# Kernel tuning notes

Measured on AMD Instinct MI355X. Metric: run time of the kernel, lower is better.

## Reference

```python
import jax, jax.numpy as jnp
import numpy as np

N_CAT, IN, HID, VOCAB, B = 512, 1536, 2048, 32000, 256
C = N_CAT + IN + HID  # cell_size = 4096


def setup_inputs() -> dict:
    key = jax.random.key(0)
    ks = jax.random.split(key, 16)
    s = 1.0 / np.sqrt(C)
    inp = {
        "category": jax.random.normal(ks[0], (B, N_CAT), jnp.float32),
        "x": jax.random.normal(ks[1], (B, IN), jnp.float32),
        "hidden": jax.random.normal(ks[2], (B, HID), jnp.float32),
        "cell": jnp.zeros((B, C), jnp.float32),
        # gate weights, torch Linear layout [out, in]
        "Wf": jax.random.uniform(ks[3], (C, C), jnp.float32, -s, s),
        "bf": jax.random.uniform(ks[4], (C,), jnp.float32, -s, s),
        "Wi": jax.random.uniform(ks[5], (C, C), jnp.float32, -s, s),
        "bi": jax.random.uniform(ks[6], (C,), jnp.float32, -s, s),
        "Wc": jax.random.uniform(ks[7], (C, C), jnp.float32, -s, s),
        "bc": jax.random.uniform(ks[8], (C,), jnp.float32, -s, s),
        "Wo": jax.random.uniform(ks[9], (C, C), jnp.float32, -s, s),
        "bo": jax.random.uniform(ks[10], (C,), jnp.float32, -s, s),
        "Wout": jax.random.uniform(ks[11], (VOCAB, C), jnp.float32, -s, s),
        "bout": jax.random.uniform(ks[12], (VOCAB,), jnp.float32, -s, s),
    }
    return inp


def reference(category, x, hidden, cell, Wf, bf, Wi, bi, Wc, bc, Wo, bo, Wout, bout):
    # concat inputs: [B, C]
    xc = jnp.concatenate([category, x, hidden], axis=1)
    # fuse the 4 gate linears into one GEMM: [B, 4C]
    Wall = jnp.concatenate([Wf, Wi, Wc, Wo], axis=0)   # [4C, C]
    ball = jnp.concatenate([bf, bi, bc, bo], axis=0)   # [4C]
    z = xc @ Wall.T + ball
    f, i, g, o = jnp.split(z, 4, axis=1)
    f = jax.nn.sigmoid(f)
    i = jax.nn.sigmoid(i)
    g = jnp.tanh(g)
    o = jax.nn.sigmoid(o)
    cell_new = f * cell + i * g                        # [B, C]
    hidden_new = o * jnp.tanh(cell_new)                # [B, C]
    out = hidden_new @ Wout.T + bout                   # [B, VOCAB]
    # dropout is identity in eval mode
    out = jax.nn.log_softmax(out, axis=1)
    return (out, cell_new, hidden_new)
```

## Files before the change

kernel.cpp:

```cpp
#include <hip/hip_runtime.h>
#include <cmath>

typedef __bf16 bf16x8 __attribute__((ext_vector_type(8)));
typedef float  f32x4  __attribute__((ext_vector_type(4)));

#define NK 64
#define ATILE 32768
#define LDS_W_OFF 32768
#define BUFB 40960

#define GLOAD_LDS16(g, l)                                                    \
    __builtin_amdgcn_global_load_lds(                                        \
        (const __attribute__((address_space(1))) unsigned int*)(g),          \
        (__attribute__((address_space(3))) unsigned int*)(l), 16, 0, 0)

__device__ __forceinline__ int swz(int row, int byteInRow) {
    return row * 128 + (byteInRow ^ ((row & 7) << 4));
}

__device__ __forceinline__ bf16x8 cvt8(f32x4 a, f32x4 b) {
    bf16x8 r;
    r[0] = (__bf16)a[0]; r[1] = (__bf16)a[1]; r[2] = (__bf16)a[2]; r[3] = (__bf16)a[3];
    r[4] = (__bf16)b[0]; r[5] = (__bf16)b[1]; r[6] = (__bf16)b[2]; r[7] = (__bf16)b[3];
    return r;
}

__global__ __launch_bounds__(256)
void prep_xc(const float* __restrict__ cat, const float* __restrict__ x,
             const float* __restrict__ hid, unsigned char* __restrict__ A0)
{
    int id  = blockIdx.x * 256 + threadIdx.x;
    int row = id >> 9, col = (id & 511) * 8;
    const float* src = (col < 512)  ? cat + (size_t)row * 512 + col
                     : (col < 2048) ? x   + (size_t)row * 1536 + (col - 512)
                                    : hid + (size_t)row * 2048 + (col - 2048);
    f32x4 a = *(const f32x4*)src, b = *(const f32x4*)(src + 4);
    int ks = col >> 6, c8 = (col & 63) >> 3;
    *(bf16x8*)(A0 + (size_t)ks * ATILE + swz(row, c8 * 16)) = cvt8(a, b);
}

template <int MODE>
__global__ __launch_bounds__(512, 4)
void gemm_bf16(const unsigned char* __restrict__ At,
               const float* __restrict__ W0, const float* __restrict__ W1,
               const float* __restrict__ W2, const float* __restrict__ W3,
               const float* __restrict__ B0, const float* __restrict__ B1,
               const float* __restrict__ B2, const float* __restrict__ B3,
               float* __restrict__ out, int ldout)
{
    __shared__ __align__(16) unsigned char lds[2 * BUFB];

    const int tid  = threadIdx.x;
    const int lane = tid & 63;
    const int wid  = tid >> 6;
    const int l15  = lane & 15;
    const int l4   = lane >> 4;
    const int wr   = wid >> 1;
    const int wc   = wid & 1;

    const int n0 = blockIdx.x * 64;
    const float* Wsrc; const float* Bsrc; int wn0;
    if (MODE == 0) {
        int g = n0 >> 12;
        Wsrc = (g == 0) ? W0 : (g == 1) ? W1 : (g == 2) ? W2 : W3;
        Bsrc = (g == 0) ? B0 : (g == 1) ? B1 : (g == 2) ? B2 : B3;
        wn0  = n0 & 4095;
    } else {
        Wsrc = W0; Bsrc = B0; wn0 = n0;
    }

    f32x4 wreg[2];
    f32x4 acc[4][2] = {};

    const int wrow = tid >> 3, wc8 = tid & 7;
    const float* wbase = Wsrc + (size_t)(wn0 + wrow) * 4096 + wc8 * 8;

    auto issueA = [&](int ks, int buf) {
        const unsigned char* src = At + (size_t)ks * ATILE + wid * 4096 + lane * 16;
        unsigned char* dst = lds + buf * BUFB + wid * 4096;
        #pragma unroll
        for (int i = 0; i < 4; ++i)
            GLOAD_LDS16(src + i * 1024, dst + i * 1024);
    };
    auto loadW  = [&](int ks) {
        const float* p = wbase + ks * 64;
        wreg[0] = *(const f32x4*)p;
        wreg[1] = *(const f32x4*)(p + 4);
    };
    auto storeW = [&](int buf) {
        *(bf16x8*)(lds + buf * BUFB + LDS_W_OFF + swz(wrow, wc8 * 16)) = cvt8(wreg[0], wreg[1]);
    };

    issueA(0, 0);
    loadW(0);
    storeW(0);
    __syncthreads();

    for (int ks = 0; ks < NK; ++ks) {
        const int cur = ks & 1;
        unsigned char* cbase = lds + cur * BUFB;
        if (ks + 1 < NK) { issueA(ks + 1, cur ^ 1); loadW(ks + 1); }
        #pragma unroll
        for (int kk = 0; kk < 2; ++kk) {
            bf16x8 af[4], bw[2];
            #pragma unroll
            for (int m = 0; m < 4; ++m) {
                int row = wr * 64 + m * 16 + l15;
                af[m] = *(const bf16x8*)(cbase + swz(row, kk * 64 + l4 * 16));
            }
            #pragma unroll
            for (int n = 0; n < 2; ++n) {
                int row = wc * 32 + n * 16 + l15;
                bw[n] = *(const bf16x8*)(cbase + LDS_W_OFF + swz(row, kk * 64 + l4 * 16));
            }
            #pragma unroll
            for (int m = 0; m < 4; ++m)
                #pragma unroll
                for (int n = 0; n < 2; ++n)
                    acc[m][n] = __builtin_amdgcn_mfma_f32_16x16x32_bf16(af[m], bw[n], acc[m][n], 0, 0, 0);
        }
        if (ks + 1 < NK) storeW(cur ^ 1);
        __syncthreads();
    }

    #pragma unroll
    for (int n = 0; n < 2; ++n) {
        int col = wc * 32 + n * 16 + l15;
        float bias = Bsrc[wn0 + col];
        #pragma unroll
        for (int m = 0; m < 4; ++m) {
            int row = wr * 64 + m * 16 + l4 * 4;
            f32x4 v = acc[m][n];
            #pragma unroll
            for (int j = 0; j < 4; ++j)
                out[(size_t)(row + j) * ldout + n0 + col] = v[j] + bias;
        }
    }
}

__global__ __launch_bounds__(256)
void lstm_elem(const float* __restrict__ z, const float* __restrict__ cell,
               float* __restrict__ cnew, float* __restrict__ hnew,
               unsigned char* __restrict__ A1)
{
    int id  = blockIdx.x * 256 + threadIdx.x;
    int row = id >> 9, col = (id & 511) * 8;
    const float* zr = z + (size_t)row * 16384 + col;
    f32x4 vf[2] = { *(const f32x4*)(zr),         *(const f32x4*)(zr + 4) };
    f32x4 vi[2] = { *(const f32x4*)(zr + 4096),  *(const f32x4*)(zr + 4100) };
    f32x4 vg[2] = { *(const f32x4*)(zr + 8192),  *(const f32x4*)(zr + 8196) };
    f32x4 vo[2] = { *(const f32x4*)(zr + 12288), *(const f32x4*)(zr + 12292) };
    const float* cr = cell + (size_t)row * 4096 + col;
    f32x4 vc[2] = { *(const f32x4*)cr, *(const f32x4*)(cr + 4) };
    f32x4 rc[2], rh[2];
    bf16x8 hb;
    #pragma unroll
    for (int h = 0; h < 2; ++h)
        #pragma unroll
        for (int j = 0; j < 4; ++j) {
            float f = 1.0f / (1.0f + __expf(-vf[h][j]));
            float i = 1.0f / (1.0f + __expf(-vi[h][j]));
            float g = tanhf(vg[h][j]);
            float o = 1.0f / (1.0f + __expf(-vo[h][j]));
            float cn = f * vc[h][j] + i * g;
            float hn = o * tanhf(cn);
            rc[h][j] = cn; rh[h][j] = hn;
            hb[h * 4 + j] = (__bf16)hn;
        }
    float* cd = cnew + (size_t)row * 4096 + col;
    float* hd = hnew + (size_t)row * 4096 + col;
    *(f32x4*)cd = rc[0]; *(f32x4*)(cd + 4) = rc[1];
    *(f32x4*)hd = rh[0]; *(f32x4*)(hd + 4) = rh[1];
    int ks = col >> 6, c8 = (col & 63) >> 3;
    *(bf16x8*)(A1 + (size_t)ks * ATILE + swz(row, c8 * 16)) = hb;
}

__global__ __launch_bounds__(256)
void logsoftmax_inplace(float* __restrict__ out)
{
    float* row    = out + (size_t)blockIdx.x * 32000;
    const int tid = threadIdx.x;
    __shared__ float redm[4], reds[4];

    float m = -1e30f, s = 0.0f;
    for (int i = tid; i < 8000; i += 256) {
        f32x4 v = *(const f32x4*)(row + i * 4);
        float t = fmaxf(fmaxf(v[0], v[1]), fmaxf(v[2], v[3]));
        float nm = fmaxf(m, t);
        s = s * __expf(m - nm) + __expf(v[0] - nm) + __expf(v[1] - nm)
                               + __expf(v[2] - nm) + __expf(v[3] - nm);
        m = nm;
    }
    #pragma unroll
    for (int off = 32; off; off >>= 1) {
        float om = __shfl_xor(m, off), os = __shfl_xor(s, off);
        float nm = fmaxf(m, om);
        s = s * __expf(m - nm) + os * __expf(om - nm);
        m = nm;
    }
    if ((tid & 63) == 0) { redm[tid >> 6] = m; reds[tid >> 6] = s; }
    __syncthreads();
    {
        float M = fmaxf(fmaxf(redm[0], redm[1]), fmaxf(redm[2], redm[3]));
        float S = reds[0] * __expf(redm[0] - M) + reds[1] * __expf(redm[1] - M)
                + reds[2] * __expf(redm[2] - M) + reds[3] * __expf(redm[3] - M);
        m = M; s = S;
    }
    float lse = m + logf(s);

    for (int i = tid; i < 8000; i += 256) {
        f32x4 v = *(const f32x4*)(row + i * 4);
        v[0] -= lse; v[1] -= lse; v[2] -= lse; v[3] -= lse;
        *(f32x4*)(row + i * 4) = v;
    }
}

extern "C" void kernel_launch(void* const* d_in, const int* in_sizes, int n_in,
                              void* d_out, int out_size, void* d_ws, size_t ws_size,
                              hipStream_t stream)
{
    const float* cat  = (const float*)d_in[0];
    const float* x    = (const float*)d_in[1];
    const float* hid  = (const float*)d_in[2];
    const float* cell = (const float*)d_in[3];
    const float* Wf   = (const float*)d_in[4];
    const float* bf   = (const float*)d_in[5];
    const float* Wi   = (const float*)d_in[6];
    const float* bi   = (const float*)d_in[7];
    const float* Wc   = (const float*)d_in[8];
    const float* bc   = (const float*)d_in[9];
    const float* Wo   = (const float*)d_in[10];
    const float* bo   = (const float*)d_in[11];
    const float* Wout = (const float*)d_in[12];
    const float* bout = (const float*)d_in[13];
    float* out = (float*)d_out;

    unsigned char* A0 = (unsigned char*)d_ws;
    unsigned char* A1 = A0 + (size_t)64 * ATILE;
    float*         z  = (float*)(A1 + (size_t)64 * ATILE);

    float* cnew = out + 8192000;
    float* hnew = out + 9240576;

    prep_xc<<<512, 256, 0, stream>>>(cat, x, hid, A0);
    gemm_bf16<0><<<256, 512, 0, stream>>>(A0, Wf, Wi, Wc, Wo, bf, bi, bc, bo, z, 16384);
    lstm_elem<<<512, 256, 0, stream>>>(z, cell, cnew, hnew, A1);
    gemm_bf16<1><<<500, 512, 0, stream>>>(A1, Wout, Wout, Wout, Wout,
                                          bout, bout, bout, bout, out, 32000);
    logsoftmax_inplace<<<256, 256, 0, stream>>>(out);
}
```

Measured before the change: 285.7 us.

## Split gate GEMM along K and deepen GEMM pipeline to two tiles in flight

The gate GEMM is split into two K halves, so the launch grows from 256 to 512 blocks, which fills more of the machine. Each half writes its own partial z buffer, and lstm_elem adds the two partials before applying the activations. Both GEMMs also now prefetch two k-steps ahead instead of one, using explicit waitcnt and barriers around that deeper prefetch. In exchange there is extra z traffic to write and read back, the workspace must be larger, and the LDS footprint grows to 80KB per block, which may limit occupancy.

```diff
diff --git a/kernel.cpp b/kernel.cpp
--- a/kernel.cpp
+++ b/kernel.cpp
@@ -4,10 +4,9 @@
 typedef __bf16 bf16x8 __attribute__((ext_vector_type(8)));
 typedef float  f32x4  __attribute__((ext_vector_type(4)));
 
-#define NK 64
 #define ATILE 32768
-#define LDS_W_OFF 32768
-#define BUFB 40960
+#define LDS_W_OFF 65536
+#define WTILE 8192
 
 #define GLOAD_LDS16(g, l)                                                    \
     __builtin_amdgcn_global_load_lds(                                        \
@@ -48,7 +47,7 @@
                const float* __restrict__ B2, const float* __restrict__ B3,
                float* __restrict__ out, int ldout)
 {
-    __shared__ __align__(16) unsigned char lds[2 * BUFB];
+    __shared__ __align__(16) unsigned char lds[2 * ATILE + 2 * WTILE];
 
     const int tid  = threadIdx.x;
     const int lane = tid & 63;
@@ -58,7 +57,16 @@
     const int wr   = wid >> 1;
     const int wc   = wid & 1;
 
-    const int n0 = blockIdx.x * 64;
+    int n0, koff, nk; float* outp;
+    if (MODE == 0) {
+        n0 = (blockIdx.x >> 1) * 64;
+        int kh = blockIdx.x & 1;
+        koff = kh * 32; nk = 32;
+        outp = out + (size_t)kh * 4194304;
+    } else {
+        n0 = blockIdx.x * 64; koff = 0; nk = 64; outp = out;
+    }
+
     const float* Wsrc; const float* Bsrc; int wn0;
     if (MODE == 0) {
         int g = n0 >> 12;
@@ -69,87 +77,114 @@
         Wsrc = W0; Bsrc = B0; wn0 = n0;
     }
 
-    f32x4 wreg[2];
+    f32x4 wreg[2][2];
     f32x4 acc[4][2] = {};
 
     const int wrow = tid >> 3, wc8 = tid & 7;
     const float* wbase = Wsrc + (size_t)(wn0 + wrow) * 4096 + wc8 * 8;
 
     auto issueA = [&](int ks, int buf) {
-        const unsigned char* src = At + (size_t)ks * ATILE + wid * 4096 + lane * 16;
-        unsigned char* dst = lds + buf * BUFB + wid * 4096;
+        const unsigned char* src = At + (size_t)(koff + ks) * ATILE + wid * 4096 + lane * 16;
+        unsigned char* dst = lds + buf * ATILE + wid * 4096;
         #pragma unroll
         for (int i = 0; i < 4; ++i)
             GLOAD_LDS16(src + i * 1024, dst + i * 1024);
     };
-    auto loadW  = [&](int ks) {
-        const float* p = wbase + ks * 64;
-        wreg[0] = *(const f32x4*)p;
-        wreg[1] = *(const f32x4*)(p + 4);
+    auto loadW = [&](int ks, int slot) {
+        const float* p = wbase + (size_t)(koff + ks) * 64;
+        wreg[slot][0] = *(const f32x4*)p;
+        wreg[slot][1] = *(const f32x4*)(p + 4);
     };
-    auto storeW = [&](int buf) {
-        *(bf16x8*)(lds + buf * BUFB + LDS_W_OFF + swz(wrow, wc8 * 16)) = cvt8(wreg[0], wreg[1]);
+    auto storeW = [&](int slot, int buf) {
+        *(bf16x8*)(lds + LDS_W_OFF + buf * WTILE + swz(wrow, wc8 * 16)) =
+            cvt8(wreg[slot][0], wreg[slot][1]);
     };
 
-    issueA(0, 0);
-    loadW(0);
-    storeW(0);
-    __syncthreads();
-
-    for (int ks = 0; ks < NK; ++ks) {
-        const int cur = ks & 1;
-        unsigned char* cbase = lds + cur * BUFB;
-        if (ks + 1 < NK) { issueA(ks + 1, cur ^ 1); loadW(ks + 1); }
+    issueA(0, 0); loadW(0, 0);
+    issueA(1, 1); loadW(1, 1);
+    asm volatile("s_waitcnt vmcnt(6)" ::: "memory");
+    __builtin_amdgcn_sched_barrier(0);
+    storeW(0, 0);
+    asm volatile("s_waitcnt lgkmcnt(0)" ::: "memory");
+    __builtin_amdgcn_s_barrier();
+
+    for (int t = 0; t < nk; ++t) {
+        const int cur = t & 1;
+        unsigned char* abase = lds + cur * ATILE;
+        unsigned char* wlds  = lds + LDS_W_OFF + cur * WTILE;
+
+        bf16x8 af[2][4], bw[2][2];
         #pragma unroll
         for (int kk = 0; kk < 2; ++kk) {
-            bf16x8 af[4], bw[2];
             #pragma unroll
             for (int m = 0; m < 4; ++m) {
                 int row = wr * 64 + m * 16 + l15;
-                af[m] = *(const bf16x8*)(cbase + swz(row, kk * 64 + l4 * 16));
+                af[kk][m] = *(const bf16x8*)(abase + swz(row, kk * 64 + l4 * 16));
             }
             #pragma unroll
             for (int n = 0; n < 2; ++n) {
                 int row = wc * 32 + n * 16 + l15;
-                bw[n] = *(const bf16x8*)(cbase + LDS_W_OFF + swz(row, kk * 64 + l4 * 16));
+                bw[kk][n] = *(const bf16x8*)(wlds + swz(row, kk * 64 + l4 * 16));
             }
+        }
+        asm volatile("s_waitcnt lgkmcnt(0)" ::: "memory");
+        __builtin_amdgcn_sched_barrier(0);
+        __builtin_amdgcn_s_barrier();
+        __builtin_amdgcn_sched_barrier(0);
+
+        if (t + 2 < nk) { issueA(t + 2, cur); loadW(t + 2, cur); }
+        #pragma unroll
+        for (int kk = 0; kk < 2; ++kk)
             #pragma unroll
             for (int m = 0; m < 4; ++m)
                 #pragma unroll
                 for (int n = 0; n < 2; ++n)
-                    acc[m][n] = __builtin_amdgcn_mfma_f32_16x16x32_bf16(af[m], bw[n], acc[m][n], 0, 0, 0);
-        }
-        if (ks + 1 < NK) storeW(cur ^ 1);
-        __syncthreads();
+                    acc[m][n] = __builtin_amdgcn_mfma_f32_16x16x32_bf16(
+                        af[kk][m], bw[kk][n], acc[m][n], 0, 0, 0);
+        if (t + 1 < nk) {
+            if (t + 2 < nk) asm volatile("s_waitcnt vmcnt(6)" ::: "memory");
+            else            asm volatile("s_waitcnt vmcnt(0)" ::: "memory");
+            __builtin_amdgcn_sched_barrier(0);
+            storeW(cur ^ 1, cur ^ 1);
+            asm volatile("s_waitcnt lgkmcnt(0)" ::: "memory");
+        }
+        __builtin_amdgcn_s_barrier();
+        __builtin_amdgcn_sched_barrier(0);
     }
 
     #pragma unroll
     for (int n = 0; n < 2; ++n) {
         int col = wc * 32 + n * 16 + l15;
-        float bias = Bsrc[wn0 + col];
+        float bias = (MODE == 1 || koff == 0) ? Bsrc[wn0 + col] : 0.0f;
         #pragma unroll
         for (int m = 0; m < 4; ++m) {
             int row = wr * 64 + m * 16 + l4 * 4;
             f32x4 v = acc[m][n];
             #pragma unroll
             for (int j = 0; j < 4; ++j)
-                out[(size_t)(row + j) * ldout + n0 + col] = v[j] + bias;
+                outp[(size_t)(row + j) * ldout + n0 + col] = v[j] + bias;
         }
     }
 }
 
 __global__ __launch_bounds__(256)
-void lstm_elem(const float* __restrict__ z, const float* __restrict__ cell,
+void lstm_elem(const float* __restrict__ z0, const float* __restrict__ z1,
+               const float* __restrict__ cell,
                float* __restrict__ cnew, float* __restrict__ hnew,
                unsigned char* __restrict__ A1)
 {
     int id  = blockIdx.x * 256 + threadIdx.x;
     int row = id >> 9, col = (id & 511) * 8;
-    const float* zr = z + (size_t)row * 16384 + col;
-    f32x4 vf[2] = { *(const f32x4*)(zr),         *(const f32x4*)(zr + 4) };
-    f32x4 vi[2] = { *(const f32x4*)(zr + 4096),  *(const f32x4*)(zr + 4100) };
-    f32x4 vg[2] = { *(const f32x4*)(zr + 8192),  *(const f32x4*)(zr + 8196) };
-    f32x4 vo[2] = { *(const f32x4*)(zr + 12288), *(const f32x4*)(zr + 12292) };
+    const float* za = z0 + (size_t)row * 16384 + col;
+    const float* zb = z1 + (size_t)row * 16384 + col;
+    f32x4 vf[2], vi[2], vg[2], vo[2];
+    #pragma unroll
+    for (int h = 0; h < 2; ++h) {
+        vf[h] = *(const f32x4*)(za + h * 4)         + *(const f32x4*)(zb + h * 4);
+        vi[h] = *(const f32x4*)(za + 4096 + h * 4)  + *(const f32x4*)(zb + 4096 + h * 4);
+        vg[h] = *(const f32x4*)(za + 8192 + h * 4)  + *(const f32x4*)(zb + 8192 + h * 4);
+        vo[h] = *(const f32x4*)(za + 12288 + h * 4) + *(const f32x4*)(zb + 12288 + h * 4);
+    }
     const float* cr = cell + (size_t)row * 4096 + col;
     f32x4 vc[2] = { *(const f32x4*)cr, *(const f32x4*)(cr + 4) };
     f32x4 rc[2], rh[2];
@@ -243,8 +278,8 @@
     float* hnew = out + 9240576;
 
     prep_xc<<<512, 256, 0, stream>>>(cat, x, hid, A0);
-    gemm_bf16<0><<<256, 512, 0, stream>>>(A0, Wf, Wi, Wc, Wo, bf, bi, bc, bo, z, 16384);
-    lstm_elem<<<512, 256, 0, stream>>>(z, cell, cnew, hnew, A1);
+    gemm_bf16<0><<<512, 512, 0, stream>>>(A0, Wf, Wi, Wc, Wo, bf, bi, bc, bo, z, 16384);
+    lstm_elem<<<512, 256, 0, stream>>>(z, z + 4194304, cell, cnew, hnew, A1);
     gemm_bf16<1><<<500, 512, 0, stream>>>(A1, Wout, Wout, Wout, Wout,
                                           bout, bout, bout, bout, out, 32000);
     logsoftmax_inplace<<<256, 256, 0, stream>>>(out);
```

Measured after the change: 287.1 us. No clear change (+0.5%).

## Fuse LSTM elementwise into gate GEMM epilogue and deepen weight-load pipeline

Applied to the files above, without the earlier changes.

The gate GEMM now gives each block 16 columns from each of the four gates, so the LSTM cell update runs in the epilogue and writes cell, hidden and the bf16 swizzled hidden tile directly. This removes the z intermediate buffer and the separate elementwise kernel. Both GEMMs switch to wider weight windows staged in registers across multiple k-steps, with explicit vmcnt/lgkmcnt waits, raw barriers and a larger 128KB LDS. The output GEMM uses 128-column tiles over 250 blocks. The larger LDS footprint lowers occupancy to 2 blocks per CU and raises register pressure, and the hand-tuned wait counts are fragile.

```diff
diff --git a/kernel.cpp b/kernel.cpp
--- a/kernel.cpp
+++ b/kernel.cpp
@@ -4,26 +4,34 @@
 typedef __bf16 bf16x8 __attribute__((ext_vector_type(8)));
 typedef float  f32x4  __attribute__((ext_vector_type(4)));
 
-#define NK 64
+template <int N> struct IC { static constexpr int v = N; };
+
 #define ATILE 32768
-#define LDS_W_OFF 32768
-#define BUFB 40960
+#define LDS_W_OFF 65536
+#define WTILE_B 32768
 
 #define GLOAD_LDS16(g, l)                                                    \
     __builtin_amdgcn_global_load_lds(                                        \
         (const __attribute__((address_space(1))) unsigned int*)(g),          \
         (__attribute__((address_space(3))) unsigned int*)(l), 16, 0, 0)
 
-__device__ __forceinline__ int swz(int row, int byteInRow) {
-    return row * 128 + (byteInRow ^ ((row & 7) << 4));
-}
-
+__device__ __forceinline__ int swz(int row, int b) {
+    return row * 128 + (b ^ ((row & 7) << 4));
+}
 __device__ __forceinline__ bf16x8 cvt8(f32x4 a, f32x4 b) {
     bf16x8 r;
     r[0] = (__bf16)a[0]; r[1] = (__bf16)a[1]; r[2] = (__bf16)a[2]; r[3] = (__bf16)a[3];
     r[4] = (__bf16)b[0]; r[5] = (__bf16)b[1]; r[6] = (__bf16)b[2]; r[7] = (__bf16)b[3];
     return r;
 }
+template <int N> __device__ __forceinline__ void waitvm() {
+    if constexpr (N == 0)  asm volatile("s_waitcnt vmcnt(0)" ::: "memory");
+    else if constexpr (N == 4)  asm volatile("s_waitcnt vmcnt(4)" ::: "memory");
+    else if constexpr (N == 12) asm volatile("s_waitcnt vmcnt(12)" ::: "memory");
+}
+__device__ __forceinline__ void waitlgkm() { asm volatile("s_waitcnt lgkmcnt(0)" ::: "memory"); }
+#define SBAR()  __builtin_amdgcn_s_barrier()
+#define SCHED() __builtin_amdgcn_sched_barrier(0)
 
 __global__ __launch_bounds__(256)
 void prep_xc(const float* __restrict__ cat, const float* __restrict__ x,
@@ -40,139 +48,187 @@
 }
 
 template <int MODE>
-__global__ __launch_bounds__(512, 4)
-void gemm_bf16(const unsigned char* __restrict__ At,
-               const float* __restrict__ W0, const float* __restrict__ W1,
-               const float* __restrict__ W2, const float* __restrict__ W3,
-               const float* __restrict__ B0, const float* __restrict__ B1,
-               const float* __restrict__ B2, const float* __restrict__ B3,
-               float* __restrict__ out, int ldout)
+__global__ __launch_bounds__(512, 2)
+void gemm_fused(const unsigned char* __restrict__ At,
+                const float* __restrict__ W0, const float* __restrict__ W1,
+                const float* __restrict__ W2, const float* __restrict__ W3,
+                const float* __restrict__ B0, const float* __restrict__ B1,
+                const float* __restrict__ B2, const float* __restrict__ B3,
+                const float* __restrict__ cell,
+                float* __restrict__ out0, float* __restrict__ out1,
+                unsigned char* __restrict__ A1out)
 {
-    __shared__ __align__(16) unsigned char lds[2 * BUFB];
+    __shared__ __align__(16) unsigned char lds[131072];
+
+    constexpr int S       = (MODE == 0) ? 4 : 2;
+    constexpr int NW      = (MODE == 0) ? 16 : 32;
+    constexpr int NKT     = 64;
+    constexpr int WIN_K   = (MODE == 0) ? 256 : 128;
+    constexpr int ROWB    = (MODE == 0) ? 512 : 256;
+    constexpr int ACC_M   = (MODE == 0) ? 2 : 4;
+    constexpr int TSTEADY = (MODE == 0) ? 56 : 60;
 
     const int tid  = threadIdx.x;
     const int lane = tid & 63;
     const int wid  = tid >> 6;
     const int l15  = lane & 15;
     const int l4   = lane >> 4;
-    const int wr   = wid >> 1;
-    const int wc   = wid & 1;
-
-    const int n0 = blockIdx.x * 64;
-    const float* Wsrc; const float* Bsrc; int wn0;
+    const int wrM  = (MODE == 0) ? wid : (wid >> 1);
+    const int wcN  = (MODE == 0) ? 0   : (wid & 1);
+
+    int c0 = 0, wn0 = 0;
+    int wrow_s, wchunk;
+    const float* wsrc;
     if (MODE == 0) {
-        int g = n0 >> 12;
-        Wsrc = (g == 0) ? W0 : (g == 1) ? W1 : (g == 2) ? W2 : W3;
-        Bsrc = (g == 0) ? B0 : (g == 1) ? B1 : (g == 2) ? B2 : B3;
-        wn0  = n0 & 4095;
+        c0 = blockIdx.x * 16;
+        wrow_s = tid >> 3; wchunk = tid & 7;
+        int gate = wrow_s >> 4;
+        const float* Wg = (gate == 0) ? W0 : (gate == 1) ? W1 : (gate == 2) ? W2 : W3;
+        wsrc = Wg + (size_t)(c0 + (wrow_s & 15)) * 4096 + wchunk * 32;
     } else {
-        Wsrc = W0; Bsrc = B0; wn0 = n0;
-    }
-
-    f32x4 wreg[2];
-    f32x4 acc[4][2] = {};
-
-    const int wrow = tid >> 3, wc8 = tid & 7;
-    const float* wbase = Wsrc + (size_t)(wn0 + wrow) * 4096 + wc8 * 8;
+        wn0 = blockIdx.x * 128;
+        wrow_s = tid >> 2; wchunk = tid & 3;
+        wsrc = W0 + (size_t)(wn0 + wrow_s) * 4096 + wchunk * 32;
+    }
+    const int sxs = (wrow_s & 7) << 4;
+
+    f32x4 wreg[2][8];
+    f32x4 acc[ACC_M][4] = {};
 
     auto issueA = [&](int ks, int buf) {
         const unsigned char* src = At + (size_t)ks * ATILE + wid * 4096 + lane * 16;
-        unsigned char* dst = lds + buf * BUFB + wid * 4096;
+        unsigned char* dst = lds + buf * ATILE + wid * 4096;
         #pragma unroll
         for (int i = 0; i < 4; ++i)
             GLOAD_LDS16(src + i * 1024, dst + i * 1024);
     };
-    auto loadW  = [&](int ks) {
-        const float* p = wbase + ks * 64;
-        wreg[0] = *(const f32x4*)p;
-        wreg[1] = *(const f32x4*)(p + 4);
-    };
-    auto storeW = [&](int buf) {
-        *(bf16x8*)(lds + buf * BUFB + LDS_W_OFF + swz(wrow, wc8 * 16)) = cvt8(wreg[0], wreg[1]);
-    };
-
-    issueA(0, 0);
-    loadW(0);
-    storeW(0);
-    __syncthreads();
-
-    for (int ks = 0; ks < NK; ++ks) {
-        const int cur = ks & 1;
-        unsigned char* cbase = lds + cur * BUFB;
-        if (ks + 1 < NK) { issueA(ks + 1, cur ^ 1); loadW(ks + 1); }
+    auto loadWwin = [&](int w, auto sl) {
+        constexpr int SL = decltype(sl)::v;
+        const float* p = wsrc + (size_t)w * WIN_K;
+        #pragma unroll
+        for (int i = 0; i < 8; ++i) wreg[SL][i] = *(const f32x4*)(p + i * 4);
+    };
+    auto storeWwin = [&](auto sl, int buf) {
+        constexpr int SL = decltype(sl)::v;
+        unsigned char* b = lds + LDS_W_OFF + buf * WTILE_B + wrow_s * ROWB;
+        const int cb = wchunk * 64;
+        *(bf16x8*)(b + ((cb +  0) ^ sxs)) = cvt8(wreg[SL][0], wreg[SL][1]);
+        *(bf16x8*)(b + ((cb + 16) ^ sxs)) = cvt8(wreg[SL][2], wreg[SL][3]);
+        *(bf16x8*)(b + ((cb + 32) ^ sxs)) = cvt8(wreg[SL][4], wreg[SL][5]);
+        *(bf16x8*)(b + ((cb + 48) ^ sxs)) = cvt8(wreg[SL][6], wreg[SL][7]);
+    };
+
+    loadWwin(0, IC<0>{});
+    waitvm<0>(); SCHED();
+    storeWwin(IC<0>{}, 0);
+    issueA(0, 0); issueA(1, 1);
+    loadWwin(1, IC<1>{});
+    waitvm<12>(); SCHED();
+    waitlgkm();
+    SBAR(); SCHED();
+
+    auto step = [&](auto tsc, auto tailc, int t0) {
+        constexpr int TS   = decltype(tsc)::v;
+        constexpr int TAIL = decltype(tailc)::v;
+        constexpr int SUB  = TS % S;
+        constexpr int ABUF = TS & 1;
+        constexpr int WB   = (TS / S) & 1;
+        const int t = t0 + TS;
+        const int w = t / S;
+        unsigned char* abase = lds + ABUF * ATILE;
+        unsigned char* wlds  = lds + LDS_W_OFF + WB * WTILE_B;
+
+        bf16x8 af[2][ACC_M], bw[2][4];
         #pragma unroll
         for (int kk = 0; kk < 2; ++kk) {
-            bf16x8 af[4], bw[2];
+            #pragma unroll
+            for (int m = 0; m < ACC_M; ++m) {
+                int row = wrM * (ACC_M * 16) + m * 16 + l15;
+                af[kk][m] = *(const bf16x8*)(abase + swz(row, kk * 64 + l4 * 16));
+            }
+            #pragma unroll
+            for (int n = 0; n < 4; ++n) {
+                int row = wcN * 64 + n * 16 + l15;
+                bw[kk][n] = *(const bf16x8*)(wlds + row * ROWB +
+                              ((SUB * 128 + kk * 64 + l4 * 16) ^ ((row & 7) << 4)));
+            }
+        }
+        waitlgkm(); SCHED();
+        SBAR(); SCHED();
+
+        if (t + 2 < NKT) issueA(t + 2, ABUF);
+        if constexpr (SUB == 0) { if (w + 2 < NW) loadWwin(w + 2, IC<WB>{}); }
+        #pragma unroll
+        for (int kk = 0; kk < 2; ++kk)
+            #pragma unroll
+            for (int m = 0; m < ACC_M; ++m)
+                #pragma unroll
+                for (int n = 0; n < 4; ++n)
+                    acc[m][n] = __builtin_amdgcn_mfma_f32_16x16x32_bf16(
+                        af[kk][m], bw[kk][n], acc[m][n], 0, 0, 0);
+        if constexpr (SUB == S - 1) {
+            if (w + 1 < NW) storeWwin(IC<WB ^ 1>{}, WB ^ 1);
+        }
+        constexpr int VM = TAIL ? ((MODE == 0) ? (TS < 6 ? 4 : 0) : (TS < 2 ? 4 : 0))
+                                : ((MODE == 0) ? ((TS & 3) < 2 ? 12 : 4) : 12);
+        waitvm<VM>(); SCHED();
+        if constexpr (SUB == S - 1) waitlgkm();
+        SBAR(); SCHED();
+    };
+
+    auto blk = [&](auto self, auto tsc, auto tailc, int t0) -> void {
+        constexpr int TS = decltype(tsc)::v;
+        step(tsc, tailc, t0);
+        if constexpr (TS + 1 < 2 * S) self(self, IC<TS + 1>{}, tailc, t0);
+    };
+    int t0 = 0;
+    for (; t0 < TSTEADY; t0 += 2 * S) blk(blk, IC<0>{}, IC<0>{}, t0);
+    blk(blk, IC<0>{}, IC<1>{}, t0);
+
+    if constexpr (MODE == 0) {
+        float* lh = (float*)lds;
+        const int ccol = c0 + l15;
+        const float bfv = B0[ccol], biv = B1[ccol], bcv = B2[ccol], bov = B3[ccol];
+        #pragma unroll
+        for (int m = 0; m < 2; ++m) {
+            #pragma unroll
+            for (int j = 0; j < 4; ++j) {
+                int row = wid * 32 + m * 16 + l4 * 4 + j;
+                float f = 1.0f / (1.0f + __expf(-(acc[m][0][j] + bfv)));
+                float i = 1.0f / (1.0f + __expf(-(acc[m][1][j] + biv)));
+                float g = tanhf(acc[m][2][j] + bcv);
+                float o = 1.0f / (1.0f + __expf(-(acc[m][3][j] + bov)));
+                float cn = f * cell[(size_t)row * 4096 + ccol] + i * g;
+                float hn = o * tanhf(cn);
+                out0[(size_t)row * 4096 + ccol] = cn;
+                out1[(size_t)row * 4096 + ccol] = hn;
+                lh[row * 16 + l15] = hn;
+            }
+        }
+        __syncthreads();
+        {
+            int row = tid >> 1, half = tid & 1;
+            const float* p = lh + row * 16 + half * 8;
+            f32x4 a = *(const f32x4*)p, b = *(const f32x4*)(p + 4);
+            int c8 = ((c0 & 63) >> 3) + half;
+            *(bf16x8*)(A1out + (size_t)(c0 >> 6) * ATILE + swz(row, c8 * 16)) = cvt8(a, b);
+        }
+    } else {
+        #pragma unroll
+        for (int n = 0; n < 4; ++n) {
+            int col = wcN * 64 + n * 16 + l15;
+            float bias = B0 ? 0.0f : 0.0f;
+            bias = B1[wn0 + col];
             #pragma unroll
             for (int m = 0; m < 4; ++m) {
-                int row = wr * 64 + m * 16 + l15;
-                af[m] = *(const bf16x8*)(cbase + swz(row, kk * 64 + l4 * 16));
+                int row = wrM * 64 + m * 16 + l4 * 4;
+                f32x4 v = acc[m][n];
+                #pragma unroll
+                for (int j = 0; j < 4; ++j)
+                    out0[(size_t)(row + j) * 32000 + wn0 + col] = v[j] + bias;
             }
-            #pragma unroll
-            for (int n = 0; n < 2; ++n) {
-                int row = wc * 32 + n * 16 + l15;
-                bw[n] = *(const bf16x8*)(cbase + LDS_W_OFF + swz(row, kk * 64 + l4 * 16));
-            }
-            #pragma unroll
-            for (int m = 0; m < 4; ++m)
-                #pragma unroll
-                for (int n = 0; n < 2; ++n)
-                    acc[m][n] = __builtin_amdgcn_mfma_f32_16x16x32_bf16(af[m], bw[n], acc[m][n], 0, 0, 0);
-        }
-        if (ks + 1 < NK) storeW(cur ^ 1);
-        __syncthreads();
-    }
-
-    #pragma unroll
-    for (int n = 0; n < 2; ++n) {
-        int col = wc * 32 + n * 16 + l15;
-        float bias = Bsrc[wn0 + col];
-        #pragma unroll
-        for (int m = 0; m < 4; ++m) {
-            int row = wr * 64 + m * 16 + l4 * 4;
-            f32x4 v = acc[m][n];
-            #pragma unroll
-            for (int j = 0; j < 4; ++j)
-                out[(size_t)(row + j) * ldout + n0 + col] = v[j] + bias;
-        }
-    }
-}
-
-__global__ __launch_bounds__(256)
-void lstm_elem(const float* __restrict__ z, const float* __restrict__ cell,
-               float* __restrict__ cnew, float* __restrict__ hnew,
-               unsigned char* __restrict__ A1)
-{
-    int id  = blockIdx.x * 256 + threadIdx.x;
-    int row = id >> 9, col = (id & 511) * 8;
-    const float* zr = z + (size_t)row * 16384 + col;
-    f32x4 vf[2] = { *(const f32x4*)(zr),         *(const f32x4*)(zr + 4) };
-    f32x4 vi[2] = { *(const f32x4*)(zr + 4096),  *(const f32x4*)(zr + 4100) };
-    f32x4 vg[2] = { *(const f32x4*)(zr + 8192),  *(const f32x4*)(zr + 8196) };
-    f32x4 vo[2] = { *(const f32x4*)(zr + 12288), *(const f32x4*)(zr + 12292) };
-    const float* cr = cell + (size_t)row * 4096 + col;
-    f32x4 vc[2] = { *(const f32x4*)cr, *(const f32x4*)(cr + 4) };
-    f32x4 rc[2], rh[2];
-    bf16x8 hb;
-    #pragma unroll
-    for (int h = 0; h < 2; ++h)
-        #pragma unroll
-        for (int j = 0; j < 4; ++j) {
-            float f = 1.0f / (1.0f + __expf(-vf[h][j]));
-            float i = 1.0f / (1.0f + __expf(-vi[h][j]));
-            float g = tanhf(vg[h][j]);
-            float o = 1.0f / (1.0f + __expf(-vo[h][j]));
-            float cn = f * vc[h][j] + i * g;
-            float hn = o * tanhf(cn);
-            rc[h][j] = cn; rh[h][j] = hn;
-            hb[h * 4 + j] = (__bf16)hn;
-        }
-    float* cd = cnew + (size_t)row * 4096 + col;
-    float* hd = hnew + (size_t)row * 4096 + col;
-    *(f32x4*)cd = rc[0]; *(f32x4*)(cd + 4) = rc[1];
-    *(f32x4*)hd = rh[0]; *(f32x4*)(hd + 4) = rh[1];
-    int ks = col >> 6, c8 = (col & 63) >> 3;
-    *(bf16x8*)(A1 + (size_t)ks * ATILE + swz(row, c8 * 16)) = hb;
+        }
+    }
 }
 
 __global__ __launch_bounds__(256)
@@ -237,15 +293,15 @@
 
     unsigned char* A0 = (unsigned char*)d_ws;
     unsigned char* A1 = A0 + (size_t)64 * ATILE;
-    float*         z  = (float*)(A1 + (size_t)64 * ATILE);
 
     float* cnew = out + 8192000;
     float* hnew = out + 9240576;
 
     prep_xc<<<512, 256, 0, stream>>>(cat, x, hid, A0);
-    gemm_bf16<0><<<256, 512, 0, stream>>>(A0, Wf, Wi, Wc, Wo, bf, bi, bc, bo, z, 16384);
-    lstm_elem<<<512, 256, 0, stream>>>(z, cell, cnew, hnew, A1);
-    gemm_bf16<1><<<500, 512, 0, stream>>>(A1, Wout, Wout, Wout, Wout,
-                                          bout, bout, bout, bout, out, 32000);
+    gemm_fused<0><<<256, 512, 0, stream>>>(A0, Wf, Wi, Wc, Wo, bf, bi, bc, bo,
+                                           cell, cnew, hnew, A1);
+    gemm_fused<1><<<250, 512, 0, stream>>>(A1, Wout, nullptr, nullptr, nullptr,
+                                           nullptr, bout, nullptr, nullptr,
+                                           nullptr, out, nullptr, nullptr);
     logsoftmax_inplace<<<256, 256, 0, stream>>>(out);
 }
```

Measured after the change: 277.9 us. 1.03x faster.

## Stream GEMM operands from registers and fuse LSTM gate math into gate GEMM

Applied to the files above, without the earlier changes.

Replaces the LDS double-buffered GEMM with a register-streaming version in which each wave loads A fragments and fp32 weight rows straight from global memory, converts weights to bf16 in registers, and software-pipelines two k-steps. The gate GEMM is reorganized so each block computes all four gates for 16 cell columns. It stages the accumulators through LDS and applies the LSTM cell update in the epilogue, which removes the z intermediate buffer and the separate elementwise kernel. The A-tile swizzle is dropped in favour of a plain row-major tile layout. The tradeoff is no LDS sharing of the weight tile across waves, so each wave re-reads weights from global or L2, and register pressure is higher.

```diff
diff --git a/kernel.cpp b/kernel.cpp
--- a/kernel.cpp
+++ b/kernel.cpp
@@ -4,19 +4,7 @@
 typedef __bf16 bf16x8 __attribute__((ext_vector_type(8)));
 typedef float  f32x4  __attribute__((ext_vector_type(4)));
 
-#define NK 64
 #define ATILE 32768
-#define LDS_W_OFF 32768
-#define BUFB 40960
-
-#define GLOAD_LDS16(g, l)                                                    \
-    __builtin_amdgcn_global_load_lds(                                        \
-        (const __attribute__((address_space(1))) unsigned int*)(g),          \
-        (__attribute__((address_space(3))) unsigned int*)(l), 16, 0, 0)
-
-__device__ __forceinline__ int swz(int row, int byteInRow) {
-    return row * 128 + (byteInRow ^ ((row & 7) << 4));
-}
 
 __device__ __forceinline__ bf16x8 cvt8(f32x4 a, f32x4 b) {
     bf16x8 r;
@@ -35,144 +23,145 @@
                      : (col < 2048) ? x   + (size_t)row * 1536 + (col - 512)
                                     : hid + (size_t)row * 2048 + (col - 2048);
     f32x4 a = *(const f32x4*)src, b = *(const f32x4*)(src + 4);
-    int ks = col >> 6, c8 = (col & 63) >> 3;
-    *(bf16x8*)(A0 + (size_t)ks * ATILE + swz(row, c8 * 16)) = cvt8(a, b);
+    *(bf16x8*)(A0 + (size_t)(col >> 6) * ATILE + row * 128 + (col & 63) * 2) = cvt8(a, b);
 }
 
 template <int MODE>
-__global__ __launch_bounds__(512, 4)
-void gemm_bf16(const unsigned char* __restrict__ At,
-               const float* __restrict__ W0, const float* __restrict__ W1,
-               const float* __restrict__ W2, const float* __restrict__ W3,
-               const float* __restrict__ B0, const float* __restrict__ B1,
-               const float* __restrict__ B2, const float* __restrict__ B3,
-               float* __restrict__ out, int ldout)
-{
-    __shared__ __align__(16) unsigned char lds[2 * BUFB];
-
+__global__ __launch_bounds__(512, 2)
+void gemm_stream(const unsigned char* __restrict__ At,
+                 const float* __restrict__ W0, const float* __restrict__ W1,
+                 const float* __restrict__ W2, const float* __restrict__ W3,
+                 const float* __restrict__ B0, const float* __restrict__ B1,
+                 const float* __restrict__ B2, const float* __restrict__ B3,
+                 const float* __restrict__ cell,
+                 float* __restrict__ out0, float* __restrict__ out1,
+                 unsigned char* __restrict__ A1out)
+{
     const int tid  = threadIdx.x;
     const int lane = tid & 63;
     const int wid  = tid >> 6;
     const int l15  = lane & 15;
     const int l4   = lane >> 4;
-    const int wr   = wid >> 1;
-    const int wc   = wid & 1;
-
-    const int n0 = blockIdx.x * 64;
-    const float* Wsrc; const float* Bsrc; int wn0;
-    if (MODE == 0) {
-        int g = n0 >> 12;
-        Wsrc = (g == 0) ? W0 : (g == 1) ? W1 : (g == 2) ? W2 : W3;
-        Bsrc = (g == 0) ? B0 : (g == 1) ? B1 : (g == 2) ? B2 : B3;
-        wn0  = n0 & 4095;
+    const int mg   = wid >> 1;
+    const int sub  = wid & 1;
+
+    const float *wp0, *wp1;
+    int c0 = 0, n0 = 0;
+    if constexpr (MODE == 0) {
+        c0 = blockIdx.x * 16;
+        const float* Wg0 = sub ? W2 : W0;
+        const float* Wg1 = sub ? W3 : W1;
+        wp0 = Wg0 + (size_t)(c0 + l15) * 4096 + l4 * 8;
+        wp1 = Wg1 + (size_t)(c0 + l15) * 4096 + l4 * 8;
     } else {
-        Wsrc = W0; Bsrc = B0; wn0 = n0;
-    }
-
-    f32x4 wreg[2];
+        n0 = blockIdx.x * 64;
+        wp0 = W0 + (size_t)(n0 + sub * 32 + l15) * 4096 + l4 * 8;
+        wp1 = wp0 + (size_t)16 * 4096;
+    }
+    const unsigned char* abase = At + (size_t)(mg * 64 + l15) * 128 + l4 * 16;
+
     f32x4 acc[4][2] = {};
 
-    const int wrow = tid >> 3, wc8 = tid & 7;
-    const float* wbase = Wsrc + (size_t)(wn0 + wrow) * 4096 + wc8 * 8;
-
-    auto issueA = [&](int ks, int buf) {
-        const unsigned char* src = At + (size_t)ks * ATILE + wid * 4096 + lane * 16;
-        unsigned char* dst = lds + buf * BUFB + wid * 4096;
-        #pragma unroll
-        for (int i = 0; i < 4; ++i)
-            GLOAD_LDS16(src + i * 1024, dst + i * 1024);
+    auto loadA = [&](int ks, bf16x8 (&af)[2][4]) {
+        const unsigned char* p = abase + (size_t)ks * ATILE;
+        #pragma unroll
+        for (int kk = 0; kk < 2; ++kk)
+            #pragma unroll
+            for (int m = 0; m < 4; ++m)
+                af[kk][m] = *(const bf16x8*)(p + m * 2048 + kk * 64);
     };
-    auto loadW  = [&](int ks) {
-        const float* p = wbase + ks * 64;
-        wreg[0] = *(const f32x4*)p;
-        wreg[1] = *(const f32x4*)(p + 4);
+    auto loadW = [&](int ks, f32x4 (&ws)[2][2][2]) {
+        #pragma unroll
+        for (int kk = 0; kk < 2; ++kk) {
+            const float* q0 = wp0 + ks * 64 + kk * 32;
+            const float* q1 = wp1 + ks * 64 + kk * 32;
+            ws[0][kk][0] = *(const f32x4*)q0;
+            ws[0][kk][1] = *(const f32x4*)(q0 + 4);
+            ws[1][kk][0] = *(const f32x4*)q1;
+            ws[1][kk][1] = *(const f32x4*)(q1 + 4);
+        }
     };
-    auto storeW = [&](int buf) {
-        *(bf16x8*)(lds + buf * BUFB + LDS_W_OFF + swz(wrow, wc8 * 16)) = cvt8(wreg[0], wreg[1]);
+    auto domfma = [&](bf16x8 (&af)[2][4], f32x4 (&ws)[2][2][2]) {
+        #pragma unroll
+        for (int kk = 0; kk < 2; ++kk) {
+            bf16x8 bw0 = cvt8(ws[0][kk][0], ws[0][kk][1]);
+            bf16x8 bw1 = cvt8(ws[1][kk][0], ws[1][kk][1]);
+            #pragma unroll
+            for (int m = 0; m < 4; ++m) {
+                acc[m][0] = __builtin_amdgcn_mfma_f32_16x16x32_bf16(af[kk][m], bw0, acc[m][0], 0, 0, 0);
+                acc[m][1] = __builtin_amdgcn_mfma_f32_16x16x32_bf16(af[kk][m], bw1, acc[m][1], 0, 0, 0);
+            }
+        }
     };
 
-    issueA(0, 0);
-    loadW(0);
-    storeW(0);
-    __syncthreads();
-
-    for (int ks = 0; ks < NK; ++ks) {
-        const int cur = ks & 1;
-        unsigned char* cbase = lds + cur * BUFB;
-        if (ks + 1 < NK) { issueA(ks + 1, cur ^ 1); loadW(ks + 1); }
-        #pragma unroll
-        for (int kk = 0; kk < 2; ++kk) {
-            bf16x8 af[4], bw[2];
+    bf16x8 afA[2][4], afB[2][4];
+    f32x4  wsA[2][2][2], wsB[2][2][2];
+    loadA(0, afA); loadW(0, wsA);
+    loadA(1, afB); loadW(1, wsB);
+    for (int ks = 0; ks < 62; ks += 2) {
+        domfma(afA, wsA);
+        loadA(ks + 2, afA); loadW(ks + 2, wsA);
+        domfma(afB, wsB);
+        loadA(ks + 3, afB); loadW(ks + 3, wsB);
+    }
+    domfma(afA, wsA);
+    domfma(afB, wsB);
+
+    if constexpr (MODE == 0) {
+        __shared__ float lsf[4 * 256 * 16];
+        #pragma unroll
+        for (int n = 0; n < 2; ++n) {
+            const int g = sub * 2 + n;
             #pragma unroll
             for (int m = 0; m < 4; ++m) {
-                int row = wr * 64 + m * 16 + l15;
-                af[m] = *(const bf16x8*)(cbase + swz(row, kk * 64 + l4 * 16));
+                const int rbase = mg * 64 + m * 16 + l4 * 4;
+                #pragma unroll
+                for (int j = 0; j < 4; ++j)
+                    lsf[(g * 256 + rbase + j) * 16 + l15] = acc[m][n][j];
             }
-            #pragma unroll
-            for (int n = 0; n < 2; ++n) {
-                int row = wc * 32 + n * 16 + l15;
-                bw[n] = *(const bf16x8*)(cbase + LDS_W_OFF + swz(row, kk * 64 + l4 * 16));
+        }
+        __syncthreads();
+        const int row = tid >> 1, ch = (tid & 1) * 8;
+        const float* cp = cell + (size_t)row * 4096 + c0 + ch;
+        f32x4 cv0 = *(const f32x4*)cp, cv1 = *(const f32x4*)(cp + 4);
+        f32x4 rc[2], rh[2]; bf16x8 hb;
+        #pragma unroll
+        for (int e = 0; e < 8; ++e) {
+            const int cidx = ch + e;
+            const float fz = lsf[(0 * 256 + row) * 16 + cidx] + B0[c0 + cidx];
+            const float iz = lsf[(1 * 256 + row) * 16 + cidx] + B1[c0 + cidx];
+            const float gz = lsf[(2 * 256 + row) * 16 + cidx] + B2[c0 + cidx];
+            const float oz = lsf[(3 * 256 + row) * 16 + cidx] + B3[c0 + cidx];
+            const float f = 1.0f / (1.0f + __expf(-fz));
+            const float i = 1.0f / (1.0f + __expf(-iz));
+            const float g = tanhf(gz);
+            const float o = 1.0f / (1.0f + __expf(-oz));
+            const float cvv = (e < 4) ? cv0[e & 3] : cv1[e & 3];
+            const float cn = f * cvv + i * g;
+            const float hn = o * tanhf(cn);
+            rc[e >> 2][e & 3] = cn; rh[e >> 2][e & 3] = hn;
+            hb[e] = (__bf16)hn;
+        }
+        float* cq = out0 + (size_t)row * 4096 + c0 + ch;
+        float* hq = out1 + (size_t)row * 4096 + c0 + ch;
+        *(f32x4*)cq = rc[0]; *(f32x4*)(cq + 4) = rc[1];
+        *(f32x4*)hq = rh[0]; *(f32x4*)(hq + 4) = rh[1];
+        *(bf16x8*)(A1out + (size_t)(c0 >> 6) * ATILE + row * 128 + ((c0 & 63) + ch) * 2) = hb;
+    } else {
+        #pragma unroll
+        for (int n = 0; n < 2; ++n) {
+            const int col = n0 + sub * 32 + n * 16 + l15;
+            const float bias = B0[col];
+            #pragma unroll
+            for (int m = 0; m < 4; ++m) {
+                const int r = mg * 64 + m * 16 + l4 * 4;
+                f32x4 v = acc[m][n];
+                #pragma unroll
+                for (int j = 0; j < 4; ++j)
+                    out0[(size_t)(r + j) * 32000 + col] = v[j] + bias;
             }
-            #pragma unroll
-            for (int m = 0; m < 4; ++m)
-                #pragma unroll
-                for (int n = 0; n < 2; ++n)
-                    acc[m][n] = __builtin_amdgcn_mfma_f32_16x16x32_bf16(af[m], bw[n], acc[m][n], 0, 0, 0);
-        }
-        if (ks + 1 < NK) storeW(cur ^ 1);
-        __syncthreads();
-    }
-
-    #pragma unroll
-    for (int n = 0; n < 2; ++n) {
-        int col = wc * 32 + n * 16 + l15;
-        float bias = Bsrc[wn0 + col];
-        #pragma unroll
-        for (int m = 0; m < 4; ++m) {
-            int row = wr * 64 + m * 16 + l4 * 4;
-            f32x4 v = acc[m][n];
-            #pragma unroll
-            for (int j = 0; j < 4; ++j)
-                out[(size_t)(row + j) * ldout + n0 + col] = v[j] + bias;
-        }
-    }
-}
-
-__global__ __launch_bounds__(256)
-void lstm_elem(const float* __restrict__ z, const float* __restrict__ cell,
-               float* __restrict__ cnew, float* __restrict__ hnew,
-               unsigned char* __restrict__ A1)
-{
-    int id  = blockIdx.x * 256 + threadIdx.x;
-    int row = id >> 9, col = (id & 511) * 8;
-    const float* zr = z + (size_t)row * 16384 + col;
-    f32x4 vf[2] = { *(const f32x4*)(zr),         *(const f32x4*)(zr + 4) };
-    f32x4 vi[2] = { *(const f32x4*)(zr + 4096),  *(const f32x4*)(zr + 4100) };
-    f32x4 vg[2] = { *(const f32x4*)(zr + 8192),  *(const f32x4*)(zr + 8196) };
-    f32x4 vo[2] = { *(const f32x4*)(zr + 12288), *(const f32x4*)(zr + 12292) };
-    const float* cr = cell + (size_t)row * 4096 + col;
-    f32x4 vc[2] = { *(const f32x4*)cr, *(const f32x4*)(cr + 4) };
-    f32x4 rc[2], rh[2];
-    bf16x8 hb;
-    #pragma unroll
-    for (int h = 0; h < 2; ++h)
-        #pragma unroll
-        for (int j = 0; j < 4; ++j) {
-            float f = 1.0f / (1.0f + __expf(-vf[h][j]));
-            float i = 1.0f / (1.0f + __expf(-vi[h][j]));
-            float g = tanhf(vg[h][j]);
-            float o = 1.0f / (1.0f + __expf(-vo[h][j]));
-            float cn = f * vc[h][j] + i * g;
-            float hn = o * tanhf(cn);
-            rc[h][j] = cn; rh[h][j] = hn;
-            hb[h * 4 + j] = (__bf16)hn;
-        }
-    float* cd = cnew + (size_t)row * 4096 + col;
-    float* hd = hnew + (size_t)row * 4096 + col;
-    *(f32x4*)cd = rc[0]; *(f32x4*)(cd + 4) = rc[1];
-    *(f32x4*)hd = rh[0]; *(f32x4*)(hd + 4) = rh[1];
-    int ks = col >> 6, c8 = (col & 63) >> 3;
-    *(bf16x8*)(A1 + (size_t)ks * ATILE + swz(row, c8 * 16)) = hb;
+        }
+    }
 }
 
 __global__ __launch_bounds__(256)
@@ -237,15 +226,15 @@
 
     unsigned char* A0 = (unsigned char*)d_ws;
     unsigned char* A1 = A0 + (size_t)64 * ATILE;
-    float*         z  = (float*)(A1 + (size_t)64 * ATILE);
 
     float* cnew = out + 8192000;
     float* hnew = out + 9240576;
 
     prep_xc<<<512, 256, 0, stream>>>(cat, x, hid, A0);
-    gemm_bf16<0><<<256, 512, 0, stream>>>(A0, Wf, Wi, Wc, Wo, bf, bi, bc, bo, z, 16384);
-    lstm_elem<<<512, 256, 0, stream>>>(z, cell, cnew, hnew, A1);
-    gemm_bf16<1><<<500, 512, 0, stream>>>(A1, Wout, Wout, Wout, Wout,
-                                          bout, bout, bout, bout, out, 32000);
+    gemm_stream<0><<<256, 512, 0, stream>>>(A0, Wf, Wi, Wc, Wo, bf, bi, bc, bo,
+                                            cell, cnew, hnew, A1);
+    gemm_stream<1><<<500, 512, 0, stream>>>(A1, Wout, nullptr, nullptr, nullptr,
+                                            bout, nullptr, nullptr, nullptr,
+                                            nullptr, out, nullptr, nullptr);
     logsoftmax_inplace<<<256, 256, 0, stream>>>(out);
 }
```

Result: slower. 739.8 us (+158.9%).
